# Optimization experiments

Measured on AMD Instinct MI355X. Metric: run time of the kernel, lower is better.

Reference implementation:

```python
import jax, jax.numpy as jnp
import numpy as np

N_NODES = 100000
N_EDGES = 1600000
IN_DIM = 128
HID_DIM = 128


def gcn_conv(x, src, dst, W, b, n_nodes):
    """PyG GCNConv: out = D^{-1/2}(A+I)D^{-1/2} (x @ W) + b.
    src/dst already include self-loops."""
    h = x @ W  # [N, out_dim]
    deg = jnp.zeros((n_nodes,), dtype=h.dtype).at[dst].add(1.0)
    dis = jnp.where(deg > 0, jax.lax.rsqrt(jnp.maximum(deg, 1.0)), 0.0)
    norm = dis[src] * dis[dst]  # [E]
    msg = h[src] * norm[:, None]  # gather + scale, [E, out_dim]
    out = jax.ops.segment_sum(msg, dst, num_segments=n_nodes)
    return out + b


def setup_inputs() -> dict:
    key = jax.random.key(0)
    k1, k2, k3, k4, k5, k6 = jax.random.split(key, 6)
    x = jax.random.normal(k1, (N_NODES, IN_DIM), dtype=jnp.float32)
    edge_index = jax.random.randint(k2, (2, N_EDGES), 0, N_NODES, dtype=jnp.int32)
    s1 = 1.0 / np.sqrt(IN_DIM)
    s2 = 1.0 / np.sqrt(HID_DIM)
    W1 = jax.random.uniform(k3, (IN_DIM, HID_DIM), jnp.float32, -s1, s1)
    b1 = jax.random.uniform(k4, (HID_DIM,), jnp.float32, -s1, s1)
    W2 = jax.random.uniform(k5, (HID_DIM, HID_DIM), jnp.float32, -s2, s2)
    b2 = jax.random.uniform(k6, (HID_DIM,), jnp.float32, -s2, s2)
    return {"x": x, "edge_index": edge_index, "W1": W1, "b1": b1, "W2": W2, "b2": b2}


def reference(x, edge_index, W1, b1, W2, b2):
    n = x.shape[0]
    loops = jnp.arange(n, dtype=edge_index.dtype)
    src = jnp.concatenate([edge_index[0], loops])
    dst = jnp.concatenate([edge_index[1], loops])
    h = jax.nn.relu(gcn_conv(x, src, dst, W1, b1, n))
    h = jax.nn.relu(gcn_conv(h, src, dst, W2, b2, n))
    # global_mean_pool with batch = arange(N): each node is its own graph,
    # so the per-graph mean is the node feature itself.
    counts = jnp.ones((n, 1), dtype=h.dtype)
    pooled = jax.ops.segment_sum(h, jnp.arange(n), num_segments=n) / counts
    return pooled
```

## Files before the change

### kernel.cpp

```cpp
#include <hip/hip_runtime.h>
#include <hip/hip_fp16.h>
#include <stdint.h>
#include <stddef.h>

#define FEAT 128
#define BKT_SHIFT 8
#define TILE 4096
#define MAXB 400
#define CAP 4608

typedef _Float16 half8 __attribute__((ext_vector_type(8)));
typedef float f32x4 __attribute__((ext_vector_type(4)));


__global__ __launch_bounds__(256) void k_initB(int* __restrict__ cursorPad, int* __restrict__ allocCtr,
                                               const float* __restrict__ W1, const float* __restrict__ W2,
                                               _Float16* __restrict__ Wt1, _Float16* __restrict__ Wt2) {
  int i = blockIdx.x * 256 + threadIdx.x;
  if (i < MAXB * 16) cursorPad[i] = 0;
  if (i == 0) allocCtr[0] = 0;
  if (i < 32768) {
    int which = i >> 14, rem = i & 16383;
    int k = rem >> 7, nn = rem & 127;
    (which ? Wt2 : Wt1)[nn * 128 + k] = (_Float16)((which ? W2 : W1)[rem]);
  }
}


__global__ __launch_bounds__(256) void k_bscatter(const int* __restrict__ src, const int* __restrict__ dst,
                                                  int* __restrict__ cursorPad, int* __restrict__ pairs,
                                                  int E, int B) {
  __shared__ int h[MAXB];
  __shared__ int cur[MAXB];
  int t0 = blockIdx.x * TILE;
  int end = min(E, t0 + TILE);
  for (int i = threadIdx.x; i < B; i += 256) h[i] = 0;
  __syncthreads();
  if (end - t0 == TILE) {
    int d[16];
#pragma unroll
    for (int k = 0; k < 16; ++k) {
      d[k] = dst[t0 + threadIdx.x + k * 256];
      atomicAdd(&h[d[k] >> BKT_SHIFT], 1);
    }
    __syncthreads();
    for (int i = threadIdx.x; i < B; i += 256)
      cur[i] = h[i] ? atomicAdd(&cursorPad[i * 16], h[i]) : 0;
    __syncthreads();
#pragma unroll
    for (int k = 0; k < 16; ++k) {
      int e = t0 + threadIdx.x + k * 256;
      int b = d[k] >> BKT_SHIFT;
      int pos = atomicAdd(&cur[b], 1);
      if (pos < CAP) pairs[b * CAP + pos] = (src[e] << 8) | (d[k] & 255);
    }
  } else {
    for (int e = t0 + threadIdx.x; e < end; e += 256) atomicAdd(&h[dst[e] >> BKT_SHIFT], 1);
    __syncthreads();
    for (int i = threadIdx.x; i < B; i += 256)
      cur[i] = h[i] ? atomicAdd(&cursorPad[i * 16], h[i]) : 0;
    __syncthreads();
    for (int e = t0 + threadIdx.x; e < end; e += 256) {
      int dd = dst[e];
      int b = dd >> BKT_SHIFT;
      int pos = atomicAdd(&cur[b], 1);
      if (pos < CAP) pairs[b * CAP + pos] = (src[e] << 8) | (dd & 255);
    }
  }
}


__global__ __launch_bounds__(256) void k_csr(const int* __restrict__ pairs, const int* __restrict__ cursorPad,
                                             int* __restrict__ cnt, int* __restrict__ rowstart,
                                             float* __restrict__ dis, int* __restrict__ allocCtr,
                                             int* __restrict__ adj, int n) {
  __shared__ int deg[256];
  __shared__ int scan[256];
  __shared__ int curs[256];
  __shared__ int base;
  int b = blockIdx.x, t = threadIdx.x;
  int nodeBase = b << BKT_SHIFT;
  int e0 = b * CAP;
  int ecnt = min(cursorPad[b * 16], CAP);
  deg[t] = 0;
  __syncthreads();
  for (int i = t; i < ecnt; i += 256) atomicAdd(&deg[pairs[e0 + i] & 255], 1);
  __syncthreads();
  int d = deg[t];
  int padded = (d + 3) & ~3;
  scan[t] = padded;
  __syncthreads();
  for (int off = 1; off < 256; off <<= 1) {
    int x = scan[t];
    int y = (t >= off) ? scan[t - off] : 0;
    __syncthreads();
    scan[t] = x + y;
    __syncthreads();
  }
  int excl = scan[t] - padded;
  if (t == 255) base = atomicAdd(allocCtr, scan[t]);
  __syncthreads();
  int rs = base + excl;
  int node = nodeBase + t;
  if (node < n) {
    rowstart[node] = rs;
    cnt[node] = d;
    dis[node] = rsqrtf((float)(d + 1));
  }
  curs[t] = rs;
  __syncthreads();
  for (int i = t; i < ecnt; i += 256) {
    int pk = pairs[e0 + i];
    int pos = atomicAdd(&curs[pk & 255], 1);
    adj[pos] = pk >> 8;
  }
}


template <bool A32>
__global__ __launch_bounds__(256, 2) void k_gemm(const void* __restrict__ Av,
                                                 const _Float16* __restrict__ Wt,
                                                 const float* __restrict__ dis,
                                                 __half* __restrict__ T, int n, int nwaves) {
  const int wid = (blockIdx.x * 256 + threadIdx.x) >> 6;
  const int lane = threadIdx.x & 63;
  const int lrow = lane & 15;
  const int lk8 = (lane >> 4) * 8;
  const int ngroups = (n + 15) >> 4;

  half8 bf[8][4];
#pragma unroll
  for (int c = 0; c < 8; ++c)
#pragma unroll
    for (int kk = 0; kk < 4; ++kk)
      bf[c][kk] = *(const half8*)(Wt + (size_t)(c * 16 + lrow) * 128 + kk * 32 + lk8);

  for (int g = wid; g < ngroups; g += nwaves) {
    int ar = g * 16 + lrow; if (ar >= n) ar = n - 1;
    half8 af[4];
    if (A32) {
      const float* arow = (const float*)Av + (size_t)ar * 128 + lk8;
#pragma unroll
      for (int kk = 0; kk < 4; ++kk) {
        float4 v0 = *(const float4*)(arow + kk * 32);
        float4 v1 = *(const float4*)(arow + kk * 32 + 4);
        af[kk] = (half8){(_Float16)v0.x, (_Float16)v0.y, (_Float16)v0.z, (_Float16)v0.w,
                         (_Float16)v1.x, (_Float16)v1.y, (_Float16)v1.z, (_Float16)v1.w};
      }
    } else {
      const _Float16* arow = (const _Float16*)Av + (size_t)ar * 128 + lk8;
#pragma unroll
      for (int kk = 0; kk < 4; ++kk) af[kk] = *(const half8*)(arow + kk * 32);
    }
    f32x4 acc[8];
#pragma unroll
    for (int c = 0; c < 8; ++c) acc[c] = (f32x4){0.f, 0.f, 0.f, 0.f};
#pragma unroll
    for (int kk = 0; kk < 4; ++kk)
#pragma unroll
      for (int c = 0; c < 8; ++c)
        acc[c] = __builtin_amdgcn_mfma_f32_16x16x32_f16(af[kk], bf[c][kk], acc[c], 0, 0, 0);
    const int r0 = g * 16 + (lane >> 4) * 4;
#pragma unroll
    for (int r = 0; r < 4; ++r) {
      int row = r0 + r;
      if (row < n) {
        float sc = dis[row];
#pragma unroll
        for (int c = 0; c < 8; ++c)
          T[(size_t)row * 128 + c * 16 + lrow] = __float2half_rn(sc * acc[c][r]);
      }
    }
  }
}


template <bool FINAL>
__global__ __launch_bounds__(256) void k_agg(const __half* __restrict__ t, const float* __restrict__ bias,
                                             const int* __restrict__ adj, const int* __restrict__ rowstart,
                                             const int* __restrict__ cnt, const float* __restrict__ dis,
                                             void* __restrict__ outV, int n) {
  int node = blockIdx.x * 4 + (threadIdx.x >> 6);
  if (node >= n) return;
  int lane = threadIdx.x & 63;
  int rs = rowstart[node];
  int d = cnt[node];
  float di = dis[node];
  float2 bb = ((const float2*)bias)[lane];
  float2 a = __half22float2(((const __half2*)(t + (size_t)node * FEAT))[lane]);
  float ax = a.x, ay = a.y;
  int p = rs, e = rs + d;
#pragma unroll 2
  for (; p + 4 <= e; p += 4) {
    int4 j4 = *(const int4*)(adj + p);
    float2 h0 = __half22float2(((const __half2*)(t + (size_t)j4.x * FEAT))[lane]);
    float2 h1 = __half22float2(((const __half2*)(t + (size_t)j4.y * FEAT))[lane]);
    float2 h2 = __half22float2(((const __half2*)(t + (size_t)j4.z * FEAT))[lane]);
    float2 h3 = __half22float2(((const __half2*)(t + (size_t)j4.w * FEAT))[lane]);
    ax += (h0.x + h1.x) + (h2.x + h3.x);
    ay += (h0.y + h1.y) + (h2.y + h3.y);
  }
  for (; p < e; ++p) {
    int j = adj[p];
    float2 hv = __half22float2(((const __half2*)(t + (size_t)j * FEAT))[lane]);
    ax += hv.x; ay += hv.y;
  }
  float vx = fmaxf(fmaf(di, ax, bb.x), 0.f);
  float vy = fmaxf(fmaf(di, ay, bb.y), 0.f);
  if (FINAL) ((float2*)((float*)outV + (size_t)node * FEAT))[lane] = make_float2(vx, vy);
  else       ((__half2*)((__half*)outV + (size_t)node * FEAT))[lane] = __floats2half2_rn(vx, vy);
}


extern "C" void kernel_launch(void* const* d_in, const int* in_sizes, int n_in,
                              void* d_out, int out_size, void* d_ws, size_t ws_size,
                              hipStream_t stream) {
  const float* x  = (const float*)d_in[0];
  const int*   ei = (const int*)d_in[1];
  const float* W1 = (const float*)d_in[2];
  const float* b1 = (const float*)d_in[3];
  const float* W2 = (const float*)d_in[4];
  const float* b2 = (const float*)d_in[5];
  float* out = (float*)d_out;

  const int n = in_sizes[0] / FEAT;
  const int E = in_sizes[1] / 2;
  const int B = (n + 255) >> BKT_SHIFT;
  const int* srcv = ei;
  const int* dstv = ei + E;

  uintptr_t p = (uintptr_t)d_ws;
  auto balloc = [&](size_t bytes) -> void* {
    void* r = (void*)p;
    p += (bytes + 255) & ~(size_t)255;
    return r;
  };
  __half*    T1   = (__half*)   balloc((size_t)n * FEAT * sizeof(__half));
  __half*    H1   = (__half*)   balloc((size_t)n * FEAT * sizeof(__half));
  __half*    T2   = (__half*)   balloc((size_t)n * FEAT * sizeof(__half));
  _Float16*  Wt1  = (_Float16*) balloc(128 * 128 * sizeof(_Float16));
  _Float16*  Wt2  = (_Float16*) balloc(128 * 128 * sizeof(_Float16));
  int*   cnt      = (int*)  balloc((size_t)n * sizeof(int));
  int*   rowstart = (int*)  balloc((size_t)n * sizeof(int));
  float* dis      = (float*)balloc((size_t)n * sizeof(float));
  int*   allocCtr = (int*)  balloc(256);
  int*   cursorPad= (int*)  balloc((size_t)MAXB * 16 * sizeof(int));
  int*   pairs    = (int*)  balloc((size_t)MAXB * CAP * sizeof(int));
  int*   adj      = (int*)  balloc(((size_t)E + 4 * (size_t)n) * sizeof(int));
  (void)ws_size; (void)n_in; (void)out_size;

  const int nb  = (n + 255) / 256;
  const int tb  = (E + TILE - 1) / TILE;
  const int ab  = (n + 3) / 4;
  const int gemmBlocks = 512;
  const int nwaves = gemmBlocks * 4;

  k_initB   <<<nb, 256, 0, stream>>>(cursorPad, allocCtr, W1, W2, Wt1, Wt2);
  k_bscatter<<<tb, 256, 0, stream>>>(srcv, dstv, cursorPad, pairs, E, B);
  k_csr     <<<B, 256, 0, stream>>>(pairs, cursorPad, cnt, rowstart, dis, allocCtr, adj, n);

  k_gemm<true>  <<<gemmBlocks, 256, 0, stream>>>(x, Wt1, dis, T1, n, nwaves);
  k_agg<false>  <<<ab, 256, 0, stream>>>(T1, b1, adj, rowstart, cnt, dis, H1, n);

  k_gemm<false> <<<gemmBlocks, 256, 0, stream>>>(H1, Wt2, dis, T2, n, nwaves);
  k_agg<true>   <<<ab, 256, 0, stream>>>(T2, b2, adj, rowstart, cnt, dis, out, n);
}
```

Baseline: 223.5 us.

## Overlap first-layer GEMM with edge bucketing in one kernel, scale in CSR pass

The first-layer x@W1 GEMM now runs inside the same launch as the edge bucket-scatter, on extra blocks, so the compute-heavy GEMM and the atomic-heavy scatter can share the GPU at the same time. Because degrees are not yet known at that point, the GEMM writes an unscaled fp16 result U1. The CSR kernel then multiplies each node row by its dis value to produce T1. This drops one launch and the serialization between the scatter and the GEMM, at the cost of an extra n×128 fp16 read and write pass and one more workspace buffer. k_initB now runs on a fixed grid of 128 blocks, which only just covers the 32768 weight-transpose elements.

```diff
diff --git a/kernel.cpp b/kernel.cpp
--- a/kernel.cpp
+++ b/kernel.cpp
@@ -19,64 +19,111 @@
   int i = blockIdx.x * 256 + threadIdx.x;
   if (i < MAXB * 16) cursorPad[i] = 0;
   if (i == 0) allocCtr[0] = 0;
-  if (i < 32768) {
-    int which = i >> 14, rem = i & 16383;
-    int k = rem >> 7, nn = rem & 127;
-    (which ? Wt2 : Wt1)[nn * 128 + k] = (_Float16)((which ? W2 : W1)[rem]);
-  }
-}
-
-
-__global__ __launch_bounds__(256) void k_bscatter(const int* __restrict__ src, const int* __restrict__ dst,
+  int which = i >> 14, rem = i & 16383;
+  int k = rem >> 7, nn = rem & 127;
+  (which ? Wt2 : Wt1)[nn * 128 + k] = (_Float16)((which ? W2 : W1)[rem]);
+}
+
+
+__global__ __launch_bounds__(256, 2) void k_build(const int* __restrict__ src, const int* __restrict__ dst,
                                                   int* __restrict__ cursorPad, int* __restrict__ pairs,
-                                                  int E, int B) {
+                                                  int E, int B, int tb,
+                                                  const float* __restrict__ x, const _Float16* __restrict__ Wt1,
+                                                  __half* __restrict__ U1, int n, int nwaves) {
   __shared__ int h[MAXB];
   __shared__ int cur[MAXB];
-  int t0 = blockIdx.x * TILE;
-  int end = min(E, t0 + TILE);
-  for (int i = threadIdx.x; i < B; i += 256) h[i] = 0;
-  __syncthreads();
-  if (end - t0 == TILE) {
-    int d[16];
-#pragma unroll
-    for (int k = 0; k < 16; ++k) {
-      d[k] = dst[t0 + threadIdx.x + k * 256];
-      atomicAdd(&h[d[k] >> BKT_SHIFT], 1);
-    }
+  if (blockIdx.x < tb) {
+    int t0 = blockIdx.x * TILE;
+    int end = min(E, t0 + TILE);
+    for (int i = threadIdx.x; i < B; i += 256) h[i] = 0;
     __syncthreads();
-    for (int i = threadIdx.x; i < B; i += 256)
-      cur[i] = h[i] ? atomicAdd(&cursorPad[i * 16], h[i]) : 0;
-    __syncthreads();
-#pragma unroll
-    for (int k = 0; k < 16; ++k) {
-      int e = t0 + threadIdx.x + k * 256;
-      int b = d[k] >> BKT_SHIFT;
-      int pos = atomicAdd(&cur[b], 1);
-      if (pos < CAP) pairs[b * CAP + pos] = (src[e] << 8) | (d[k] & 255);
+    if (end - t0 == TILE) {
+      int d[16];
+#pragma unroll
+      for (int k = 0; k < 16; ++k) {
+        d[k] = dst[t0 + threadIdx.x + k * 256];
+        atomicAdd(&h[d[k] >> BKT_SHIFT], 1);
+      }
+      __syncthreads();
+      for (int i = threadIdx.x; i < B; i += 256)
+        cur[i] = h[i] ? atomicAdd(&cursorPad[i * 16], h[i]) : 0;
+      __syncthreads();
+#pragma unroll
+      for (int k = 0; k < 16; ++k) {
+        int e = t0 + threadIdx.x + k * 256;
+        int b = d[k] >> BKT_SHIFT;
+        int pos = atomicAdd(&cur[b], 1);
+        if (pos < CAP) pairs[b * CAP + pos] = (src[e] << 8) | (d[k] & 255);
+      }
+    } else {
+      for (int e = t0 + threadIdx.x; e < end; e += 256) atomicAdd(&h[dst[e] >> BKT_SHIFT], 1);
+      __syncthreads();
+      for (int i = threadIdx.x; i < B; i += 256)
+        cur[i] = h[i] ? atomicAdd(&cursorPad[i * 16], h[i]) : 0;
+      __syncthreads();
+      for (int e = t0 + threadIdx.x; e < end; e += 256) {
+        int dd = dst[e];
+        int b = dd >> BKT_SHIFT;
+        int pos = atomicAdd(&cur[b], 1);
+        if (pos < CAP) pairs[b * CAP + pos] = (src[e] << 8) | (dd & 255);
+      }
     }
   } else {
-    for (int e = t0 + threadIdx.x; e < end; e += 256) atomicAdd(&h[dst[e] >> BKT_SHIFT], 1);
-    __syncthreads();
-    for (int i = threadIdx.x; i < B; i += 256)
-      cur[i] = h[i] ? atomicAdd(&cursorPad[i * 16], h[i]) : 0;
-    __syncthreads();
-    for (int e = t0 + threadIdx.x; e < end; e += 256) {
-      int dd = dst[e];
-      int b = dd >> BKT_SHIFT;
-      int pos = atomicAdd(&cur[b], 1);
-      if (pos < CAP) pairs[b * CAP + pos] = (src[e] << 8) | (dd & 255);
+    const int wid = ((blockIdx.x - tb) * 256 + threadIdx.x) >> 6;
+    const int lane = threadIdx.x & 63;
+    const int lrow = lane & 15;
+    const int lk8 = (lane >> 4) * 8;
+    const int ngroups = (n + 15) >> 4;
+
+    half8 bf[8][4];
+#pragma unroll
+    for (int c = 0; c < 8; ++c)
+#pragma unroll
+      for (int kk = 0; kk < 4; ++kk)
+        bf[c][kk] = *(const half8*)(Wt1 + (size_t)(c * 16 + lrow) * 128 + kk * 32 + lk8);
+
+    for (int g = wid; g < ngroups; g += nwaves) {
+      int ar = g * 16 + lrow; if (ar >= n) ar = n - 1;
+      const float* arow = x + (size_t)ar * 128 + lk8;
+      half8 af[4];
+#pragma unroll
+      for (int kk = 0; kk < 4; ++kk) {
+        float4 v0 = *(const float4*)(arow + kk * 32);
+        float4 v1 = *(const float4*)(arow + kk * 32 + 4);
+        af[kk] = (half8){(_Float16)v0.x, (_Float16)v0.y, (_Float16)v0.z, (_Float16)v0.w,
+                         (_Float16)v1.x, (_Float16)v1.y, (_Float16)v1.z, (_Float16)v1.w};
+      }
+      f32x4 acc[8];
+#pragma unroll
+      for (int c = 0; c < 8; ++c) acc[c] = (f32x4){0.f, 0.f, 0.f, 0.f};
+#pragma unroll
+      for (int kk = 0; kk < 4; ++kk)
+#pragma unroll
+        for (int c = 0; c < 8; ++c)
+          acc[c] = __builtin_amdgcn_mfma_f32_16x16x32_f16(af[kk], bf[c][kk], acc[c], 0, 0, 0);
+      const int r0 = g * 16 + (lane >> 4) * 4;
+#pragma unroll
+      for (int r = 0; r < 4; ++r) {
+        int row = r0 + r;
+        if (row < n)
+#pragma unroll
+          for (int c = 0; c < 8; ++c)
+            U1[(size_t)row * 128 + c * 16 + lrow] = __float2half_rn(acc[c][r]);
+      }
     }
   }
 }
 
 
-__global__ __launch_bounds__(256) void k_csr(const int* __restrict__ pairs, const int* __restrict__ cursorPad,
-                                             int* __restrict__ cnt, int* __restrict__ rowstart,
-                                             float* __restrict__ dis, int* __restrict__ allocCtr,
-                                             int* __restrict__ adj, int n) {
+__global__ __launch_bounds__(256) void k_csrT(const int* __restrict__ pairs, const int* __restrict__ cursorPad,
+                                              int* __restrict__ cnt, int* __restrict__ rowstart,
+                                              float* __restrict__ dis, int* __restrict__ allocCtr,
+                                              int* __restrict__ adj,
+                                              const __half* __restrict__ U1, __half* __restrict__ T1, int n) {
   __shared__ int deg[256];
   __shared__ int scan[256];
   __shared__ int curs[256];
+  __shared__ float disS[256];
   __shared__ int base;
   int b = blockIdx.x, t = threadIdx.x;
   int nodeBase = b << BKT_SHIFT;
@@ -91,10 +138,10 @@
   scan[t] = padded;
   __syncthreads();
   for (int off = 1; off < 256; off <<= 1) {
-    int x = scan[t];
+    int xg = scan[t];
     int y = (t >= off) ? scan[t - off] : 0;
     __syncthreads();
-    scan[t] = x + y;
+    scan[t] = xg + y;
     __syncthreads();
   }
   int excl = scan[t] - padded;
@@ -102,10 +149,12 @@
   __syncthreads();
   int rs = base + excl;
   int node = nodeBase + t;
+  float dv = rsqrtf((float)(d + 1));
+  disS[t] = dv;
   if (node < n) {
     rowstart[node] = rs;
     cnt[node] = d;
-    dis[node] = rsqrtf((float)(d + 1));
+    dis[node] = dv;
   }
   curs[t] = rs;
   __syncthreads();
@@ -114,14 +163,21 @@
     int pos = atomicAdd(&curs[pk & 255], 1);
     adj[pos] = pk >> 8;
   }
-}
-
-
-template <bool A32>
-__global__ __launch_bounds__(256, 2) void k_gemm(const void* __restrict__ Av,
-                                                 const _Float16* __restrict__ Wt,
-                                                 const float* __restrict__ dis,
-                                                 __half* __restrict__ T, int n, int nwaves) {
+  for (int idx = t; idx < 256 * 64; idx += 256) {
+    int r = idx >> 6, c = idx & 63;
+    int nd = nodeBase + r;
+    if (nd >= n) continue;
+    float di = disS[r];
+    float2 v = __half22float2(((const __half2*)(U1 + (size_t)nd * FEAT))[c]);
+    ((__half2*)(T1 + (size_t)nd * FEAT))[c] = __floats2half2_rn(di * v.x, di * v.y);
+  }
+}
+
+
+__global__ __launch_bounds__(256, 2) void k_gemm2(const __half* __restrict__ Av,
+                                                  const _Float16* __restrict__ Wt,
+                                                  const float* __restrict__ dis,
+                                                  __half* __restrict__ T, int n, int nwaves) {
   const int wid = (blockIdx.x * 256 + threadIdx.x) >> 6;
   const int lane = threadIdx.x & 63;
   const int lrow = lane & 15;
@@ -137,21 +193,10 @@
 
   for (int g = wid; g < ngroups; g += nwaves) {
     int ar = g * 16 + lrow; if (ar >= n) ar = n - 1;
+    const _Float16* arow = (const _Float16*)Av + (size_t)ar * 128 + lk8;
     half8 af[4];
-    if (A32) {
-      const float* arow = (const float*)Av + (size_t)ar * 128 + lk8;
-#pragma unroll
-      for (int kk = 0; kk < 4; ++kk) {
-        float4 v0 = *(const float4*)(arow + kk * 32);
-        float4 v1 = *(const float4*)(arow + kk * 32 + 4);
-        af[kk] = (half8){(_Float16)v0.x, (_Float16)v0.y, (_Float16)v0.z, (_Float16)v0.w,
-                         (_Float16)v1.x, (_Float16)v1.y, (_Float16)v1.z, (_Float16)v1.w};
-      }
-    } else {
-      const _Float16* arow = (const _Float16*)Av + (size_t)ar * 128 + lk8;
-#pragma unroll
-      for (int kk = 0; kk < 4; ++kk) af[kk] = *(const half8*)(arow + kk * 32);
-    }
+#pragma unroll
+    for (int kk = 0; kk < 4; ++kk) af[kk] = *(const half8*)(arow + kk * 32);
     f32x4 acc[8];
 #pragma unroll
     for (int c = 0; c < 8; ++c) acc[c] = (f32x4){0.f, 0.f, 0.f, 0.f};
@@ -235,6 +280,7 @@
     p += (bytes + 255) & ~(size_t)255;
     return r;
   };
+  __half*    U1   = (__half*)   balloc((size_t)n * FEAT * sizeof(__half));
   __half*    T1   = (__half*)   balloc((size_t)n * FEAT * sizeof(__half));
   __half*    H1   = (__half*)   balloc((size_t)n * FEAT * sizeof(__half));
   __half*    T2   = (__half*)   balloc((size_t)n * FEAT * sizeof(__half));
@@ -249,19 +295,17 @@
   int*   adj      = (int*)  balloc(((size_t)E + 4 * (size_t)n) * sizeof(int));
   (void)ws_size; (void)n_in; (void)out_size;
 
-  const int nb  = (n + 255) / 256;
   const int tb  = (E + TILE - 1) / TILE;
   const int ab  = (n + 3) / 4;
   const int gemmBlocks = 512;
   const int nwaves = gemmBlocks * 4;
 
-  k_initB   <<<nb, 256, 0, stream>>>(cursorPad, allocCtr, W1, W2, Wt1, Wt2);
-  k_bscatter<<<tb, 256, 0, stream>>>(srcv, dstv, cursorPad, pairs, E, B);
-  k_csr     <<<B, 256, 0, stream>>>(pairs, cursorPad, cnt, rowstart, dis, allocCtr, adj, n);
-
-  k_gemm<true>  <<<gemmBlocks, 256, 0, stream>>>(x, Wt1, dis, T1, n, nwaves);
-  k_agg<false>  <<<ab, 256, 0, stream>>>(T1, b1, adj, rowstart, cnt, dis, H1, n);
-
-  k_gemm<false> <<<gemmBlocks, 256, 0, stream>>>(H1, Wt2, dis, T2, n, nwaves);
-  k_agg<true>   <<<ab, 256, 0, stream>>>(T2, b2, adj, rowstart, cnt, dis, out, n);
-}
+  k_initB <<<128, 256, 0, stream>>>(cursorPad, allocCtr, W1, W2, Wt1, Wt2);
+  k_build <<<tb + gemmBlocks, 256, 0, stream>>>(srcv, dstv, cursorPad, pairs, E, B, tb,
+                                                x, Wt1, U1, n, nwaves);
+  k_csrT  <<<B, 256, 0, stream>>>(pairs, cursorPad, cnt, rowstart, dis, allocCtr, adj, U1, T1, n);
+
+  k_agg<false> <<<ab, 256, 0, stream>>>(T1, b1, adj, rowstart, cnt, dis, H1, n);
+  k_gemm2      <<<gemmBlocks, 256, 0, stream>>>(H1, Wt2, dis, T2, n, nwaves);
+  k_agg<true>  <<<ab, 256, 0, stream>>>(T2, b2, adj, rowstart, cnt, dis, out, n);
+}
```

Result: slower. 235.1 us (+5.2%).

## Stage bucket scatter and CSR build in shared memory for coalesced writes

Applied to the files above, without the earlier changes.

The bucket-scatter kernel now counts edges per bucket, sorts them locally by bucket in LDS and then writes them to the global pairs array in contiguous runs. This replaces scattered per-edge global stores. The CSR kernel loads each bucket's pairs into LDS once, swaps the block-wide scan with __syncthreads for a wave-shuffle scan, and writes adj contiguously from an LDS staging buffer. The cost is much larger LDS use per block (32KB+ in bscatter, about 40KB in csr), which may reduce occupancy. These preprocessing kernels are a small part of total time next to the GEMM and aggregation kernels.

```diff
diff --git a/kernel.cpp b/kernel.cpp
--- a/kernel.cpp
+++ b/kernel.cpp
@@ -8,6 +8,7 @@
 #define TILE 4096
 #define MAXB 400
 #define CAP 4608
+#define PADMAX (CAP + 768)
 
 typedef _Float16 half8 __attribute__((ext_vector_type(8)));
 typedef float f32x4 __attribute__((ext_vector_type(4)));
@@ -19,11 +20,9 @@
   int i = blockIdx.x * 256 + threadIdx.x;
   if (i < MAXB * 16) cursorPad[i] = 0;
   if (i == 0) allocCtr[0] = 0;
-  if (i < 32768) {
-    int which = i >> 14, rem = i & 16383;
-    int k = rem >> 7, nn = rem & 127;
-    (which ? Wt2 : Wt1)[nn * 128 + k] = (_Float16)((which ? W2 : W1)[rem]);
-  }
+  int which = i >> 14, rem = i & 16383;
+  int k = rem >> 7, nn = rem & 127;
+  (which ? Wt2 : Wt1)[nn * 128 + k] = (_Float16)((which ? W2 : W1)[rem]);
 }
 
 
@@ -31,40 +30,70 @@
                                                   int* __restrict__ cursorPad, int* __restrict__ pairs,
                                                   int E, int B) {
   __shared__ int h[MAXB];
+  __shared__ int lbase[MAXB];
   __shared__ int cur[MAXB];
+  __shared__ int hcnt[MAXB];
+  __shared__ int staged[TILE];
+  __shared__ int dests[TILE];
+  const int tid = threadIdx.x;
   int t0 = blockIdx.x * TILE;
-  int end = min(E, t0 + TILE);
-  for (int i = threadIdx.x; i < B; i += 256) h[i] = 0;
-  __syncthreads();
-  if (end - t0 == TILE) {
-    int d[16];
+  int cnt = min(E - t0, TILE);
+
+  for (int i = tid; i < B; i += 256) h[i] = 0;
+  __syncthreads();
+
+  if (cnt == TILE) {
+    int d[16], s_[16];
 #pragma unroll
     for (int k = 0; k < 16; ++k) {
-      d[k] = dst[t0 + threadIdx.x + k * 256];
+      d[k] = dst[t0 + tid + k * 256];
+      s_[k] = src[t0 + tid + k * 256];
       atomicAdd(&h[d[k] >> BKT_SHIFT], 1);
     }
     __syncthreads();
-    for (int i = threadIdx.x; i < B; i += 256)
+    if (tid < 64) {
+      int l = tid, b7 = l * 7;
+      int v[7]; int sum = 0;
+#pragma unroll
+      for (int q = 0; q < 7; ++q) { int b = b7 + q; v[q] = (b < B) ? h[b] : 0; sum += v[q]; }
+      int incl = sum;
+      for (int off = 1; off < 64; off <<= 1) { int y = __shfl_up(incl, off); if (l >= off) incl += y; }
+      int run = incl - sum;
+#pragma unroll
+      for (int q = 0; q < 7; ++q) { int b = b7 + q; if (b < B) lbase[b] = run; run += v[q]; }
+    }
+    for (int i = tid; i < B; i += 256) {
       cur[i] = h[i] ? atomicAdd(&cursorPad[i * 16], h[i]) : 0;
+      hcnt[i] = 0;
+    }
     __syncthreads();
 #pragma unroll
     for (int k = 0; k < 16; ++k) {
-      int e = t0 + threadIdx.x + k * 256;
       int b = d[k] >> BKT_SHIFT;
-      int pos = atomicAdd(&cur[b], 1);
-      if (pos < CAP) pairs[b * CAP + pos] = (src[e] << 8) | (d[k] & 255);
+      int r = atomicAdd(&hcnt[b], 1);
+      int li = lbase[b] + r;
+      int pos = cur[b] + r;
+      staged[li] = (s_[k] << 8) | (d[k] & 255);
+      dests[li] = (pos < CAP) ? (b * CAP + pos) : -1;
+    }
+    __syncthreads();
+    for (int i = tid; i < TILE; i += 256) {
+      int dd = dests[i];
+      if (dd >= 0) pairs[dd] = staged[i];
     }
   } else {
-    for (int e = t0 + threadIdx.x; e < end; e += 256) atomicAdd(&h[dst[e] >> BKT_SHIFT], 1);
-    __syncthreads();
-    for (int i = threadIdx.x; i < B; i += 256)
+    for (int e = tid; e < cnt; e += 256) atomicAdd(&h[dst[t0 + e] >> BKT_SHIFT], 1);
+    __syncthreads();
+    for (int i = tid; i < B; i += 256) {
       cur[i] = h[i] ? atomicAdd(&cursorPad[i * 16], h[i]) : 0;
-    __syncthreads();
-    for (int e = t0 + threadIdx.x; e < end; e += 256) {
-      int dd = dst[e];
+      hcnt[i] = 0;
+    }
+    __syncthreads();
+    for (int e = tid; e < cnt; e += 256) {
+      int dd = dst[t0 + e];
       int b = dd >> BKT_SHIFT;
-      int pos = atomicAdd(&cur[b], 1);
-      if (pos < CAP) pairs[b * CAP + pos] = (src[e] << 8) | (dd & 255);
+      int pos = cur[b] + atomicAdd(&hcnt[b], 1);
+      if (pos < CAP) pairs[b * CAP + pos] = (src[t0 + e] << 8) | (dd & 255);
     }
   }
 }
@@ -74,46 +103,51 @@
                                              int* __restrict__ cnt, int* __restrict__ rowstart,
                                              float* __restrict__ dis, int* __restrict__ allocCtr,
                                              int* __restrict__ adj, int n) {
+  __shared__ int pr[CAP];
+  __shared__ int stagedAdj[PADMAX];
   __shared__ int deg[256];
-  __shared__ int scan[256];
-  __shared__ int curs[256];
-  __shared__ int base;
-  int b = blockIdx.x, t = threadIdx.x;
-  int nodeBase = b << BKT_SHIFT;
-  int e0 = b * CAP;
-  int ecnt = min(cursorPad[b * 16], CAP);
+  __shared__ int lcur[256];
+  __shared__ int wsum[4];
+  __shared__ int sbase;
+  const int b = blockIdx.x, t = threadIdx.x;
+  const int w = t >> 6, lane = t & 63;
+  const int nodeBase = b << BKT_SHIFT;
+  const int e0 = b * CAP;
+  const int ecnt = min(cursorPad[b * 16], CAP);
+
   deg[t] = 0;
-  __syncthreads();
-  for (int i = t; i < ecnt; i += 256) atomicAdd(&deg[pairs[e0 + i] & 255], 1);
-  __syncthreads();
+  for (int i = t; i < ecnt; i += 256) pr[i] = pairs[e0 + i];
+  __syncthreads();
+  for (int i = t; i < ecnt; i += 256) atomicAdd(&deg[pr[i] & 255], 1);
+  __syncthreads();
+
   int d = deg[t];
   int padded = (d + 3) & ~3;
-  scan[t] = padded;
-  __syncthreads();
-  for (int off = 1; off < 256; off <<= 1) {
-    int x = scan[t];
-    int y = (t >= off) ? scan[t - off] : 0;
-    __syncthreads();
-    scan[t] = x + y;
-    __syncthreads();
-  }
-  int excl = scan[t] - padded;
-  if (t == 255) base = atomicAdd(allocCtr, scan[t]);
-  __syncthreads();
-  int rs = base + excl;
+  int incl = padded;
+  for (int off = 1; off < 64; off <<= 1) { int y = __shfl_up(incl, off); if (lane >= off) incl += y; }
+  if (lane == 63) wsum[w] = incl;
+  __syncthreads();
+  int tot  = wsum[0] + wsum[1] + wsum[2] + wsum[3];
+  int woff = (w > 0 ? wsum[0] : 0) + (w > 1 ? wsum[1] : 0) + (w > 2 ? wsum[2] : 0);
+  int excl = woff + incl - padded;
+  if (t == 0) sbase = atomicAdd(allocCtr, tot);
+  lcur[t] = excl;
+  __syncthreads();
+
+  int base = sbase;
   int node = nodeBase + t;
   if (node < n) {
-    rowstart[node] = rs;
+    rowstart[node] = base + excl;
     cnt[node] = d;
     dis[node] = rsqrtf((float)(d + 1));
   }
-  curs[t] = rs;
-  __syncthreads();
   for (int i = t; i < ecnt; i += 256) {
-    int pk = pairs[e0 + i];
-    int pos = atomicAdd(&curs[pk & 255], 1);
-    adj[pos] = pk >> 8;
-  }
+    int pk = pr[i];
+    int li = atomicAdd(&lcur[pk & 255], 1);
+    stagedAdj[li] = pk >> 8;
+  }
+  __syncthreads();
+  for (int i = t; i < tot; i += 256) adj[base + i] = stagedAdj[i];
 }
 
 
@@ -249,13 +283,12 @@
   int*   adj      = (int*)  balloc(((size_t)E + 4 * (size_t)n) * sizeof(int));
   (void)ws_size; (void)n_in; (void)out_size;
 
-  const int nb  = (n + 255) / 256;
   const int tb  = (E + TILE - 1) / TILE;
   const int ab  = (n + 3) / 4;
   const int gemmBlocks = 512;
   const int nwaves = gemmBlocks * 4;
 
-  k_initB   <<<nb, 256, 0, stream>>>(cursorPad, allocCtr, W1, W2, Wt1, Wt2);
+  k_initB   <<<128, 256, 0, stream>>>(cursorPad, allocCtr, W1, W2, Wt1, Wt2);
   k_bscatter<<<tb, 256, 0, stream>>>(srcv, dstv, cursorPad, pairs, E, B);
   k_csr     <<<B, 256, 0, stream>>>(pairs, cursorPad, cnt, rowstart, dis, allocCtr, adj, n);
 
```

After: 212.9 us. -4.8%, faster.
